# Optimization experiments

Hardware: AMD Instinct MI355X
Metric: run time of the kernel (lower is better)

## Reference

```python
import jax, jax.numpy as jnp
import numpy as np

SCALE = 16.0
TEMP = 0.07
EPS = 1e-8


def setup_inputs() -> dict:
    key = jax.random.key(0)
    k0, k1, k2, k3, k4 = jax.random.split(key, 5)
    B, D, h, w = 16, 128, 48, 48
    feats_a = jax.random.normal(k0, (B, D, h, w), jnp.float32)
    feats_b = jax.random.normal(k1, (B, D, h, w), jnp.float32)
    eye = jnp.eye(3, dtype=jnp.float32)
    # near-identity homographies (must be invertible)
    Hs_a = eye[None] + 0.02 * jax.random.normal(k2, (B, 3, 3), jnp.float32)
    Hs_b = eye[None] + 0.02 * jax.random.normal(k3, (B, 3, 3), jnp.float32)
    # near-identity affine with a small translation (in large-image pixels)
    M_a_b = jnp.array([[1.0, 0.0, 24.0], [0.0, 1.0, -16.0]], jnp.float32) \
        + 0.01 * jax.random.normal(k4, (2, 3), jnp.float32)
    return {"feats_a": feats_a, "feats_b": feats_b, "Hs_a": Hs_a, "Hs_b": Hs_b, "M_a_b": M_a_b}


def _transform_matrix(Hs_a, Hs_b, M_a_b):
    # Feat_A -> Img_A -> Large_A -> Large_B -> Img_B -> Feat_B
    B = Hs_a.shape[0]
    dt = Hs_a.dtype
    M3 = jnp.concatenate([M_a_b, jnp.array([[0.0, 0.0, 1.0]], dt)], axis=0)  # (3,3)
    S = jnp.diag(jnp.array([SCALE, SCALE, 1.0], dt))
    S_inv = jnp.diag(jnp.array([1.0 / SCALE, 1.0 / SCALE, 1.0], dt))
    Ha_inv = jnp.linalg.inv(Hs_a)  # (B,3,3)
    T = S_inv[None] @ Hs_b @ M3[None] @ Ha_inv @ S[None]
    return T


def _bilinear_sample(feats, grid):
    # feats (B,D,H,W); grid (B,h,w,2) normalized to [-1,1], align_corners=True,
    # zero padding for out-of-range samples (matches F.grid_sample).
    B, D, H, W = feats.shape
    h, w = grid.shape[1], grid.shape[2]
    ix = (grid[..., 0] + 1.0) * 0.5 * (W - 1)  # (B,h,w)
    iy = (grid[..., 1] + 1.0) * 0.5 * (H - 1)
    x0 = jnp.floor(ix); y0 = jnp.floor(iy)
    wx1 = ix - x0; wx0 = 1.0 - wx1
    wy1 = iy - y0; wy0 = 1.0 - wy1
    feats_flat = feats.reshape(B, D, H * W)

    def gather(xi, yi):
        valid = (xi >= 0) & (xi <= W - 1) & (yi >= 0) & (yi <= H - 1)
        xc = jnp.clip(xi, 0, W - 1).astype(jnp.int32)
        yc = jnp.clip(yi, 0, H - 1).astype(jnp.int32)
        idx = (yc * W + xc).reshape(B, -1)  # (B, h*w)
        v = jnp.take_along_axis(feats_flat, idx[:, None, :], axis=2)  # (B,D,h*w)
        return v * valid.reshape(B, 1, -1).astype(feats.dtype)

    out = (gather(x0, y0) * (wx0 * wy0).reshape(B, 1, -1)
           + gather(x0 + 1, y0) * (wx1 * wy0).reshape(B, 1, -1)
           + gather(x0, y0 + 1) * (wx0 * wy1).reshape(B, 1, -1)
           + gather(x0 + 1, y0 + 1) * (wx1 * wy1).reshape(B, 1, -1))
    return out.reshape(B, D, h, w)


def reference(feats_a, feats_b, Hs_a, Hs_b, M_a_b):
    B, D, h, w = feats_a.shape
    N = h * w
    H_b, W_b = feats_b.shape[2], feats_b.shape[3]
    T = _transform_matrix(Hs_a, Hs_b, M_a_b)  # (B,3,3)

    # homogeneous pixel grid of feats_a: (3, N)
    gy, gx = jnp.meshgrid(jnp.arange(h, dtype=jnp.float32), jnp.arange(w, dtype=jnp.float32), indexing='ij')
    coords = jnp.stack([gx.ravel(), gy.ravel(), jnp.ones(N, jnp.float32)], axis=0)  # (3,N)
    new = jnp.einsum('bij,jn->bin', T, coords)  # (B,3,N)
    z = new[:, 2, :] + EPS
    x_norm = 2.0 * (new[:, 0, :] / z) / (W_b - 1) - 1.0  # (B,N)
    y_norm = 2.0 * (new[:, 1, :] / z) / (H_b - 1) - 1.0
    grid = jnp.stack([x_norm, y_norm], axis=-1).reshape(B, h, w, 2)
    valid_mask = ((grid[..., 0] >= -1) & (grid[..., 0] <= 1)
                  & (grid[..., 1] >= -1) & (grid[..., 1] <= 1)).astype(jnp.float32)  # (B,h,w)

    warped_b = _bilinear_sample(feats_b, grid)  # (B,D,h,w)

    fa = feats_a.reshape(B, D, N).transpose(0, 2, 1)   # (B,N,D)
    wb = warped_b.reshape(B, D, N).transpose(0, 2, 1)  # (B,N,D)
    # F.normalize: x / max(||x||, eps) with eps=1e-12
    fa = fa / jnp.maximum(jnp.linalg.norm(fa, axis=2, keepdims=True), 1e-12)
    wb = wb / jnp.maximum(jnp.linalg.norm(wb, axis=2, keepdims=True), 1e-12)

    logits = jnp.einsum('bnd,bmd->bnm', fa, wb) / TEMP  # (B,N,N)
    # cross-entropy with labels = diagonal
    lse = jax.nn.logsumexp(logits, axis=-1)  # (B,N)
    diag = jnp.einsum('bnn->bn', logits)     # (B,N)
    loss_per = lse - diag                    # (B,N)

    mask = valid_mask.reshape(B, N)
    num_valid = mask.sum()
    total = (loss_per * mask).sum()
    return jnp.where(num_valid > 0, total / jnp.maximum(num_valid, 1.0), 0.0)
```

## Files before the change

### kernel.cpp

```cpp
#include <hip/hip_runtime.h>
#include <math.h>

#define B_ 16
#define D_ 128
#define HH 48
#define WW 48
#define N_ 2304
#define NC 72
#define SCALE_ 16.0f
#define INV_TEMP 14.285714285714286f
#define L2E_TEMP 20.60992915555662f
#define EPS_ 1e-8f
#define SPLITC 6
#define STAGES 6

typedef __attribute__((ext_vector_type(8))) short bf16x8;
typedef __attribute__((ext_vector_type(16))) float f32x16;

__device__ __forceinline__ short f2bf(float f) {
    union { float f; unsigned u; } v; v.f = f;
    unsigned r = v.u + 0x7FFFu + ((v.u >> 16) & 1u);
    return (short)(r >> 16);
}

__device__ __forceinline__ size_t frag_off(int b, int c, int ks, int lane) {
    return ((((size_t)b * NC + c) * 8 + ks) << 9) + (size_t)lane * 8;
}

__device__ __forceinline__ void gld16(const short* g, short* l) {
    __builtin_amdgcn_global_load_lds(
        (const __attribute__((address_space(1))) void*)g,
        (__attribute__((address_space(3))) void*)l, 16, 0, 0);
}

__global__ __launch_bounds__(256) void k_prep(const float* __restrict__ fa,
                                              const float* __restrict__ fb,
                                              const float* __restrict__ Ha,
                                              const float* __restrict__ Hb,
                                              const float* __restrict__ Mab,
                                              float* __restrict__ maskA,
                                              short* __restrict__ faF,
                                              short* __restrict__ wbF) {
    __shared__ float part[4][2][32];
    const int b = blockIdx.y;
    const int rb = blockIdx.x;
    const int n0 = rb * 32;
    const int tid = threadIdx.x;
    const int lane = tid & 63, wv = tid >> 6;
    const int r = lane & 31, h = lane >> 5;
    const int n = n0 + r;

    float T[9];
    {
        const float* A = Ha + b * 9;
        const float* Bm = Hb + b * 9;
        float c00 = A[4] * A[8] - A[5] * A[7];
        float c01 = A[5] * A[6] - A[3] * A[8];
        float c02 = A[3] * A[7] - A[4] * A[6];
        float id = 1.f / (A[0] * c00 + A[1] * c01 + A[2] * c02);
        float inv[9] = { c00 * id, (A[2] * A[7] - A[1] * A[8]) * id, (A[1] * A[5] - A[2] * A[4]) * id,
                         c01 * id, (A[0] * A[8] - A[2] * A[6]) * id, (A[2] * A[3] - A[0] * A[5]) * id,
                         c02 * id, (A[1] * A[6] - A[0] * A[7]) * id, (A[0] * A[4] - A[1] * A[3]) * id };
        float M3[9] = {Mab[0], Mab[1], Mab[2], Mab[3], Mab[4], Mab[5], 0.f, 0.f, 1.f};
        float P1[9], P2[9];
        for (int i = 0; i < 3; ++i)
            for (int j = 0; j < 3; ++j) {
                float s = 0.f;
                for (int k = 0; k < 3; ++k) s += Bm[i * 3 + k] * M3[k * 3 + j];
                P1[i * 3 + j] = s;
            }
        for (int i = 0; i < 3; ++i)
            for (int j = 0; j < 3; ++j) {
                float s = 0.f;
                for (int k = 0; k < 3; ++k) s += P1[i * 3 + k] * inv[k * 3 + j];
                P2[i * 3 + j] = s;
            }
        const float sc[3] = {SCALE_, SCALE_, 1.f};
        for (int i = 0; i < 3; ++i)
            for (int j = 0; j < 3; ++j) T[i * 3 + j] = P2[i * 3 + j] * sc[j] / sc[i];
    }

    const float gx = (float)(n % WW), gy = (float)(n / WW);
    const float X = T[0] * gx + T[1] * gy + T[2];
    const float Y = T[3] * gx + T[4] * gy + T[5];
    const float z = T[6] * gx + T[7] * gy + T[8] + EPS_;
    const float xn = 2.f * (X / z) / (float)(WW - 1) - 1.f;
    const float yn = 2.f * (Y / z) / (float)(HH - 1) - 1.f;
    const float msk = (xn >= -1.f && xn <= 1.f && yn >= -1.f && yn <= 1.f) ? 1.f : 0.f;
    const float ix = (xn + 1.f) * 0.5f * (float)(WW - 1);
    const float iy = (yn + 1.f) * 0.5f * (float)(HH - 1);
    const float x0f = floorf(ix), y0f = floorf(iy);
    const float wx1 = ix - x0f, wx0 = 1.f - wx1;
    const float wy1 = iy - y0f, wy0 = 1.f - wy1;
    const bool vx0 = (x0f >= 0.f) && (x0f <= 47.f);
    const bool vx1 = (x0f + 1.f >= 0.f) && (x0f + 1.f <= 47.f);
    const bool vy0 = (y0f >= 0.f) && (y0f <= 47.f);
    const bool vy1 = (y0f + 1.f >= 0.f) && (y0f + 1.f <= 47.f);
    const float w00 = (vx0 && vy0) ? wx0 * wy0 : 0.f;
    const float w01 = (vx1 && vy0) ? wx1 * wy0 : 0.f;
    const float w10 = (vx0 && vy1) ? wx0 * wy1 : 0.f;
    const float w11 = (vx1 && vy1) ? wx1 * wy1 : 0.f;
    const int x0c = (int)fminf(fmaxf(x0f, 0.f), 47.f);
    const int x1c = (int)fminf(fmaxf(x0f + 1.f, 0.f), 47.f);
    const int y0c = (int)fminf(fmaxf(y0f, 0.f), 47.f);
    const int y1c = (int)fminf(fmaxf(y0f + 1.f, 0.f), 47.f);
    const int o00 = y0c * WW + x0c, o01 = y0c * WW + x1c;
    const int o10 = y1c * WW + x0c, o11 = y1c * WW + x1c;

    const float* fab = fa + (size_t)b * D_ * N_;
    const float* fbb = fb + (size_t)b * D_ * N_;

    float av[2][8], wvv[2][8];
    float sA = 0.f, sW = 0.f;
    #pragma unroll
    for (int g = 0; g < 2; ++g) {
        const int ks = wv + 4 * g;
        const int dbase = ks * 16 + h * 8;
        #pragma unroll
        for (int j = 0; j < 8; ++j) {
            const int d = dbase + j;
            const float* p = fbb + (size_t)d * N_;
            float w = w00 * p[o00] + w01 * p[o01] + w10 * p[o10] + w11 * p[o11];
            float a = fab[(size_t)d * N_ + n];
            av[g][j] = a; wvv[g][j] = w;
            sA += a * a; sW += w * w;
        }
    }
    sA += __shfl_xor(sA, 32);
    sW += __shfl_xor(sW, 32);
    if (lane < 32) { part[wv][0][r] = sA; part[wv][1][r] = sW; }
    if (tid < 32) maskA[b * N_ + n0 + r] = msk;
    __syncthreads();
    const float rnA = 1.f / fmaxf(sqrtf(part[0][0][r] + part[1][0][r] + part[2][0][r] + part[3][0][r]), 1e-12f);
    const float rnW = 1.f / fmaxf(sqrtf(part[0][1][r] + part[1][1][r] + part[2][1][r] + part[3][1][r]), 1e-12f);

    #pragma unroll
    for (int g = 0; g < 2; ++g) {
        const int ks = wv + 4 * g;
        bf16x8 oa, ow;
        #pragma unroll
        for (int j = 0; j < 8; ++j) {
            oa[j] = f2bf(av[g][j] * rnA);
            ow[j] = f2bf(wvv[g][j] * rnW);
        }
        size_t off = frag_off(b, rb, ks, lane);
        *(bf16x8*)(faF + off) = oa;
        *(bf16x8*)(wbF + off) = ow;
    }
}

__global__ __launch_bounds__(256, 4) void k_loss(const short* __restrict__ faF,
                                                 const short* __restrict__ wbF,
                                                 float* __restrict__ Zpart,
                                                 float* __restrict__ dgbuf) {
    __shared__ short bbuf[2][8192];
    __shared__ float s_Z[128];
    const int lin = blockIdx.x;
    const int xcd = lin & 7;
    const int i0 = lin >> 3;
    const int b = xcd * 2 + (i0 / 108);
    const int r108 = i0 % 108;
    const int bx = r108 % 18;
    const int cs = r108 / 18;
    const int tid = threadIdx.x;
    const int lane = tid & 63, w = tid >> 6;
    const int l31 = lane & 31, h = lane >> 5;
    const int rc = bx * 4 + w;

    bf16x8 af[8];
    #pragma unroll
    for (int ks = 0; ks < 8; ++ks)
        af[ks] = *(const bf16x8*)(faF + frag_off(b, rc, ks, lane));

    float Z[16];
    #pragma unroll
    for (int i = 0; i < 16; ++i) Z[i] = 0.f;

    const short* bsrc = wbF + frag_off(b, cs * 12, 0, 0);

    #define STAGE_B(nb, s) { \
        const short* sg = bsrc + (size_t)(s) * 8192 + w * 2048 + lane * 8; \
        short* sl = &bbuf[nb][w * 2048]; \
        _Pragma("unroll") \
        for (int j = 0; j < 4; ++j) gld16(sg + j * 512, sl + j * 512); \
    }

    STAGE_B(0, 0);
    STAGE_B(1, 1);
    asm volatile("s_waitcnt vmcnt(4)" ::: "memory");
    __builtin_amdgcn_sched_barrier(0);
    __builtin_amdgcn_s_barrier();

    for (int s = 0; s < STAGES; ++s) {
        const short* bb = &bbuf[s & 1][0];
        f32x16 C0, C1;
        #pragma unroll
        for (int i = 0; i < 16; ++i) { C0[i] = 0.f; C1[i] = 0.f; }
        __builtin_amdgcn_s_setprio(1);
        #pragma unroll
        for (int ks = 0; ks < 8; ++ks) {
            bf16x8 b0 = *(const bf16x8*)(bb + ks * 512 + lane * 8);
            bf16x8 b1 = *(const bf16x8*)(bb + 4096 + ks * 512 + lane * 8);
            C0 = __builtin_amdgcn_mfma_f32_32x32x16_bf16(af[ks], b0, C0, 0, 0, 0);
            C1 = __builtin_amdgcn_mfma_f32_32x32x16_bf16(af[ks], b1, C1, 0, 0, 0);
        }
        __builtin_amdgcn_s_setprio(0);
        #pragma unroll
        for (int i = 0; i < 16; ++i) {
            Z[i] += exp2f(fmaf(C0[i], L2E_TEMP, -L2E_TEMP))
                  + exp2f(fmaf(C1[i], L2E_TEMP, -L2E_TEMP));
        }
        const int jc0 = cs * 12 + 2 * s, jc1 = jc0 + 1;
        if (jc0 == rc) {
            #pragma unroll
            for (int i = 0; i < 16; ++i) {
                int rr = (i & 3) + 8 * (i >> 2) + 4 * h;
                if (l31 == rr) dgbuf[b * N_ + rc * 32 + rr] = INV_TEMP * C0[i];
            }
        }
        if (jc1 == rc) {
            #pragma unroll
            for (int i = 0; i < 16; ++i) {
                int rr = (i & 3) + 8 * (i >> 2) + 4 * h;
                if (l31 == rr) dgbuf[b * N_ + rc * 32 + rr] = INV_TEMP * C1[i];
            }
        }
        asm volatile("" ::: "memory");
        __builtin_amdgcn_s_barrier();
        if (s + 2 < STAGES) STAGE_B(s & 1, s + 2);
        if (s + 1 < STAGES) {
            if (s + 2 < STAGES) { asm volatile("s_waitcnt vmcnt(4)" ::: "memory"); }
            else               { asm volatile("s_waitcnt vmcnt(0)" ::: "memory"); }
            __builtin_amdgcn_sched_barrier(0);
        }
        asm volatile("" ::: "memory");
        __builtin_amdgcn_s_barrier();
    }
    #undef STAGE_B

    #pragma unroll
    for (int i = 0; i < 16; ++i) {
        float z = Z[i];
        z += __shfl_xor(z, 1);
        z += __shfl_xor(z, 2);
        z += __shfl_xor(z, 4);
        z += __shfl_xor(z, 8);
        z += __shfl_xor(z, 16);
        if (l31 == 0) {
            int rr = (i & 3) + 8 * (i >> 2) + 4 * h;
            s_Z[w * 32 + rr] = z;
        }
    }
    __syncthreads();
    if (tid < 128)
        Zpart[((size_t)cs * B_ + b) * N_ + bx * 128 + tid] = s_Z[tid];
}

__global__ __launch_bounds__(256) void k_pass2(const float* __restrict__ maskA,
                                               const float* __restrict__ Zpart,
                                               const float* __restrict__ dgbuf,
                                               float* __restrict__ partials) {
    const int idx = blockIdx.x * 256 + threadIdx.x;
    float Zs = 0.f;
    #pragma unroll
    for (int s = 0; s < SPLITC; ++s) Zs += Zpart[(size_t)s * B_ * N_ + idx];
    const float m = maskA[idx];
    float lossv = (logf(Zs) + INV_TEMP - dgbuf[idx]) * m;
    float cm = m;
    for (int off = 1; off < 64; off <<= 1) {
        lossv += __shfl_xor(lossv, off);
        cm += __shfl_xor(cm, off);
    }
    __shared__ float s[8];
    const int wv = threadIdx.x >> 6;
    if ((threadIdx.x & 63) == 0) { s[wv * 2] = lossv; s[wv * 2 + 1] = cm; }
    __syncthreads();
    if (threadIdx.x == 0) {
        partials[blockIdx.x * 2] = s[0] + s[2] + s[4] + s[6];
        partials[blockIdx.x * 2 + 1] = s[1] + s[3] + s[5] + s[7];
    }
}

__global__ void k_final(const float* __restrict__ partials, float* __restrict__ out) {
    const int t = threadIdx.x;
    float tt = 0.f, cc = 0.f;
    for (int i = t; i < 144; i += 64) { tt += partials[i * 2]; cc += partials[i * 2 + 1]; }
    for (int off = 1; off < 64; off <<= 1) {
        tt += __shfl_xor(tt, off);
        cc += __shfl_xor(cc, off);
    }
    if (t == 0) out[0] = (cc > 0.f) ? tt / fmaxf(cc, 1.f) : 0.f;
}

extern "C" void kernel_launch(void* const* d_in, const int* in_sizes, int n_in,
                              void* d_out, int out_size, void* d_ws, size_t ws_size,
                              hipStream_t stream) {
    const float* fa = (const float*)d_in[0];
    const float* fb = (const float*)d_in[1];
    const float* Ha = (const float*)d_in[2];
    const float* Hb = (const float*)d_in[3];
    const float* M = (const float*)d_in[4];
    float* out = (float*)d_out;

    float* wsf = (float*)d_ws;
    float* Zpart = wsf;
    float* dgbuf = Zpart + (size_t)SPLITC * B_ * N_;
    float* maskA = dgbuf + B_ * N_;
    float* partials = maskA + B_ * N_;
    short* faF = (short*)(partials + 512);
    short* wbF = faF + (size_t)B_ * NC * 8 * 512;

    hipLaunchKernelGGL(k_prep, dim3(NC, B_), dim3(256), 0, stream,
                       fa, fb, Ha, Hb, M, maskA, faF, wbF);
    hipLaunchKernelGGL(k_loss, dim3(8 * 216), dim3(256), 0, stream,
                       faF, wbF, Zpart, dgbuf);
    hipLaunchKernelGGL(k_pass2, dim3(B_ * N_ / 256), dim3(256), 0, stream,
                       maskA, Zpart, dgbuf, partials);
    hipLaunchKernelGGL(k_final, dim3(1), dim3(64), 0, stream, partials, out);
}
```

Before: 137.3 us.

## Software-pipeline MFMA stage with deferred exp/softmax accumulation of previous stage

```diff
diff --git a/kernel.cpp b/kernel.cpp
--- a/kernel.cpp
+++ b/kernel.cpp
@@ -185,58 +185,75 @@
         for (int j = 0; j < 4; ++j) gld16(sg + j * 512, sl + j * 512); \
     }
 
+    #define MFMA_STAGE(s, C0v, C1v) { \
+        const short* bb = &bbuf[(s) & 1][0]; \
+        _Pragma("unroll") \
+        for (int i = 0; i < 16; ++i) { C0v[i] = 0.f; C1v[i] = 0.f; } \
+        __builtin_amdgcn_s_setprio(1); \
+        _Pragma("unroll") \
+        for (int ks = 0; ks < 8; ++ks) { \
+            bf16x8 b0 = *(const bf16x8*)(bb + ks * 512 + lane * 8); \
+            bf16x8 b1 = *(const bf16x8*)(bb + 4096 + ks * 512 + lane * 8); \
+            C0v = __builtin_amdgcn_mfma_f32_32x32x16_bf16(af[ks], b0, C0v, 0, 0, 0); \
+            C1v = __builtin_amdgcn_mfma_f32_32x32x16_bf16(af[ks], b1, C1v, 0, 0, 0); \
+        } \
+        __builtin_amdgcn_s_setprio(0); \
+    }
+
+    #define SM_STAGE(sp, C0v, C1v) { \
+        _Pragma("unroll") \
+        for (int i = 0; i < 16; ++i) { \
+            Z[i] += exp2f(fmaf(C0v[i], L2E_TEMP, -L2E_TEMP)) \
+                  + exp2f(fmaf(C1v[i], L2E_TEMP, -L2E_TEMP)); \
+        } \
+        const int jc0 = cs * 12 + 2 * (sp), jc1 = jc0 + 1; \
+        if (jc0 == rc) { \
+            _Pragma("unroll") \
+            for (int i = 0; i < 16; ++i) { \
+                int rr = (i & 3) + 8 * (i >> 2) + 4 * h; \
+                if (l31 == rr) dgbuf[b * N_ + rc * 32 + rr] = INV_TEMP * C0v[i]; \
+            } \
+        } \
+        if (jc1 == rc) { \
+            _Pragma("unroll") \
+            for (int i = 0; i < 16; ++i) { \
+                int rr = (i & 3) + 8 * (i >> 2) + 4 * h; \
+                if (l31 == rr) dgbuf[b * N_ + rc * 32 + rr] = INV_TEMP * C1v[i]; \
+            } \
+        } \
+    }
+
+    f32x16 Ca0, Ca1, Cb0, Cb1;
+
     STAGE_B(0, 0);
     STAGE_B(1, 1);
     asm volatile("s_waitcnt vmcnt(4)" ::: "memory");
     __builtin_amdgcn_sched_barrier(0);
     __builtin_amdgcn_s_barrier();
 
+    #pragma unroll
     for (int s = 0; s < STAGES; ++s) {
-        const short* bb = &bbuf[s & 1][0];
-        f32x16 C0, C1;
-        #pragma unroll
-        for (int i = 0; i < 16; ++i) { C0[i] = 0.f; C1[i] = 0.f; }
-        __builtin_amdgcn_s_setprio(1);
-        #pragma unroll
-        for (int ks = 0; ks < 8; ++ks) {
-            bf16x8 b0 = *(const bf16x8*)(bb + ks * 512 + lane * 8);
-            bf16x8 b1 = *(const bf16x8*)(bb + 4096 + ks * 512 + lane * 8);
-            C0 = __builtin_amdgcn_mfma_f32_32x32x16_bf16(af[ks], b0, C0, 0, 0, 0);
-            C1 = __builtin_amdgcn_mfma_f32_32x32x16_bf16(af[ks], b1, C1, 0, 0, 0);
-        }
-        __builtin_amdgcn_s_setprio(0);
-        #pragma unroll
-        for (int i = 0; i < 16; ++i) {
-            Z[i] += exp2f(fmaf(C0[i], L2E_TEMP, -L2E_TEMP))
-                  + exp2f(fmaf(C1[i], L2E_TEMP, -L2E_TEMP));
-        }
-        const int jc0 = cs * 12 + 2 * s, jc1 = jc0 + 1;
-        if (jc0 == rc) {
-            #pragma unroll
-            for (int i = 0; i < 16; ++i) {
-                int rr = (i & 3) + 8 * (i >> 2) + 4 * h;
-                if (l31 == rr) dgbuf[b * N_ + rc * 32 + rr] = INV_TEMP * C0[i];
-            }
-        }
-        if (jc1 == rc) {
-            #pragma unroll
-            for (int i = 0; i < 16; ++i) {
-                int rr = (i & 3) + 8 * (i >> 2) + 4 * h;
-                if (l31 == rr) dgbuf[b * N_ + rc * 32 + rr] = INV_TEMP * C1[i];
-            }
-        }
+        if ((s & 1) == 0) { MFMA_STAGE(s, Ca0, Ca1); }
+        else              { MFMA_STAGE(s, Cb0, Cb1); }
         asm volatile("" ::: "memory");
         __builtin_amdgcn_s_barrier();
         if (s + 2 < STAGES) STAGE_B(s & 1, s + 2);
+        if (s > 0) {
+            if ((s & 1) == 0) { SM_STAGE(s - 1, Cb0, Cb1); }
+            else              { SM_STAGE(s - 1, Ca0, Ca1); }
+        }
         if (s + 1 < STAGES) {
             if (s + 2 < STAGES) { asm volatile("s_waitcnt vmcnt(4)" ::: "memory"); }
-            else               { asm volatile("s_waitcnt vmcnt(0)" ::: "memory"); }
+            else                { asm volatile("s_waitcnt vmcnt(0)" ::: "memory"); }
             __builtin_amdgcn_sched_barrier(0);
         }
         asm volatile("" ::: "memory");
         __builtin_amdgcn_s_barrier();
     }
+    SM_STAGE(STAGES - 1, Cb0, Cb1);
     #undef STAGE_B
+    #undef MFMA_STAGE
+    #undef SM_STAGE
 
     #pragma unroll
     for (int i = 0; i < 16; ++i) {
```

New measurement: 512.7 us. 3.73x slower.

## Transpose feats_b to channel-last so bilinear gathers use vector loads

Applied to the files above, without the earlier changes.

```diff
diff --git a/kernel.cpp b/kernel.cpp
--- a/kernel.cpp
+++ b/kernel.cpp
@@ -33,8 +33,33 @@
         (__attribute__((address_space(3))) void*)l, 16, 0, 0);
 }
 
+__global__ __launch_bounds__(256) void k_tr(const float* __restrict__ fb,
+                                            float* __restrict__ fbT) {
+    __shared__ float t[128][68];
+    const int b = blockIdx.y;
+    const int n0 = blockIdx.x * 64;
+    const int tid = threadIdx.x;
+    const float* src = fb + (size_t)b * D_ * N_;
+    float* dst = fbT + (size_t)b * N_ * D_;
+    #pragma unroll
+    for (int it = 0; it < 8; ++it) {
+        const int d = it * 16 + (tid >> 4);
+        const int nn = 4 * (tid & 15);
+        float4 v = *(const float4*)(src + (size_t)d * N_ + n0 + nn);
+        *(float4*)(&t[d][nn]) = v;
+    }
+    __syncthreads();
+    #pragma unroll
+    for (int it = 0; it < 8; ++it) {
+        const int nn = it * 8 + (tid >> 5);
+        const int d = 4 * (tid & 31);
+        float4 v = { t[d][nn], t[d + 1][nn], t[d + 2][nn], t[d + 3][nn] };
+        *(float4*)(dst + (size_t)(n0 + nn) * D_ + d) = v;
+    }
+}
+
 __global__ __launch_bounds__(256) void k_prep(const float* __restrict__ fa,
-                                              const float* __restrict__ fb,
+                                              const float* __restrict__ fbT,
                                               const float* __restrict__ Ha,
                                               const float* __restrict__ Hb,
                                               const float* __restrict__ Mab,
@@ -108,7 +133,11 @@
     const int o10 = y1c * WW + x0c, o11 = y1c * WW + x1c;
 
     const float* fab = fa + (size_t)b * D_ * N_;
-    const float* fbb = fb + (size_t)b * D_ * N_;
+    const float* fbtb = fbT + (size_t)b * N_ * D_;
+    const float* p00 = fbtb + (size_t)o00 * D_;
+    const float* p01 = fbtb + (size_t)o01 * D_;
+    const float* p10 = fbtb + (size_t)o10 * D_;
+    const float* p11 = fbtb + (size_t)o11 * D_;
 
     float av[2][8], wvv[2][8];
     float sA = 0.f, sW = 0.f;
@@ -116,14 +145,25 @@
     for (int g = 0; g < 2; ++g) {
         const int ks = wv + 4 * g;
         const int dbase = ks * 16 + h * 8;
+        float4 c00a = *(const float4*)(p00 + dbase), c00b = *(const float4*)(p00 + dbase + 4);
+        float4 c01a = *(const float4*)(p01 + dbase), c01b = *(const float4*)(p01 + dbase + 4);
+        float4 c10a = *(const float4*)(p10 + dbase), c10b = *(const float4*)(p10 + dbase + 4);
+        float4 c11a = *(const float4*)(p11 + dbase), c11b = *(const float4*)(p11 + dbase + 4);
+        float cw[8];
+        cw[0] = w00 * c00a.x + w01 * c01a.x + w10 * c10a.x + w11 * c11a.x;
+        cw[1] = w00 * c00a.y + w01 * c01a.y + w10 * c10a.y + w11 * c11a.y;
+        cw[2] = w00 * c00a.z + w01 * c01a.z + w10 * c10a.z + w11 * c11a.z;
+        cw[3] = w00 * c00a.w + w01 * c01a.w + w10 * c10a.w + w11 * c11a.w;
+        cw[4] = w00 * c00b.x + w01 * c01b.x + w10 * c10b.x + w11 * c11b.x;
+        cw[5] = w00 * c00b.y + w01 * c01b.y + w10 * c10b.y + w11 * c11b.y;
+        cw[6] = w00 * c00b.z + w01 * c01b.z + w10 * c10b.z + w11 * c11b.z;
+        cw[7] = w00 * c00b.w + w01 * c01b.w + w10 * c10b.w + w11 * c11b.w;
         #pragma unroll
         for (int j = 0; j < 8; ++j) {
             const int d = dbase + j;
-            const float* p = fbb + (size_t)d * N_;
-            float w = w00 * p[o00] + w01 * p[o01] + w10 * p[o10] + w11 * p[o11];
             float a = fab[(size_t)d * N_ + n];
-            av[g][j] = a; wvv[g][j] = w;
-            sA += a * a; sW += w * w;
+            av[g][j] = a; wvv[g][j] = cw[j];
+            sA += a * a; sW += cw[j] * cw[j];
         }
     }
     sA += __shfl_xor(sA, 32);
@@ -309,9 +349,11 @@
     float* partials = maskA + B_ * N_;
     short* faF = (short*)(partials + 512);
     short* wbF = faF + (size_t)B_ * NC * 8 * 512;
-
+    float* fbT = (float*)(wbF + (size_t)B_ * NC * 8 * 512);
+
+    hipLaunchKernelGGL(k_tr, dim3(N_ / 64, B_), dim3(256), 0, stream, fb, fbT);
     hipLaunchKernelGGL(k_prep, dim3(NC, B_), dim3(256), 0, stream,
-                       fa, fb, Ha, Hb, M, maskA, faF, wbF);
+                       fa, fbT, Ha, Hb, M, maskA, faF, wbF);
     hipLaunchKernelGGL(k_loss, dim3(8 * 216), dim3(256), 0, stream,
                        faF, wbF, Zpart, dgbuf);
     hipLaunchKernelGGL(k_pass2, dim3(B_ * N_ / 256), dim3(256), 0, stream,
```

New measurement: 134.7 us. Within noise of the previous version (-1.9%).
